# Optimization experiments

Measured on AMD Instinct MI355X. Metric: run time of the kernel, lower is better.

Reference implementation:

```python
import jax, jax.numpy as jnp
import numpy as np

B, N, M = 4, 4096, 1024
QUERY_DIM, CONTEXT_DIM = 1024, 768
HEADS, DIM_HEAD = 16, 64
INNER = HEADS * DIM_HEAD  # 1024


def setup_inputs() -> dict:
    key = jax.random.key(0)
    ks = jax.random.split(key, 7)
    s_q = 1.0 / np.sqrt(QUERY_DIM)
    s_c = 1.0 / np.sqrt(CONTEXT_DIM)
    s_i = 1.0 / np.sqrt(INNER)
    return {
        "x": jax.random.normal(ks[0], (B, N, QUERY_DIM), dtype=jnp.float32),
        "context": jax.random.normal(ks[1], (B, M, CONTEXT_DIM), dtype=jnp.float32),
        # weights stored [in, out] so y = x @ W (equiv to torch Linear with W.T)
        "Wq": jax.random.uniform(ks[2], (QUERY_DIM, INNER), minval=-s_q, maxval=s_q, dtype=jnp.float32),
        "Wk": jax.random.uniform(ks[3], (CONTEXT_DIM, INNER), minval=-s_c, maxval=s_c, dtype=jnp.float32),
        "Wv": jax.random.uniform(ks[4], (CONTEXT_DIM, INNER), minval=-s_c, maxval=s_c, dtype=jnp.float32),
        "Wo": jax.random.uniform(ks[5], (INNER, QUERY_DIM), minval=-s_i, maxval=s_i, dtype=jnp.float32),
        "bo": jax.random.uniform(ks[6], (QUERY_DIM,), minval=-s_i, maxval=s_i, dtype=jnp.float32),
    }


def reference(x, context, Wq, Wk, Wv, Wo, bo):
    scale = DIM_HEAD ** -0.5
    b, n, _ = x.shape
    m = context.shape[1]
    # projections, then split heads: [B, H, S, Dh]
    q = (x @ Wq).reshape(b, n, HEADS, DIM_HEAD).transpose(0, 2, 1, 3)
    k = (context @ Wk).reshape(b, m, HEADS, DIM_HEAD).transpose(0, 2, 1, 3)
    v = (context @ Wv).reshape(b, m, HEADS, DIM_HEAD).transpose(0, 2, 1, 3)
    sim = jnp.einsum('bhid,bhjd->bhij', q, k) * scale  # [B,H,N,M]
    attn = jax.nn.softmax(sim, axis=-1)
    out = jnp.einsum('bhij,bhjd->bhid', attn, v)       # [B,H,N,Dh]
    out = out.transpose(0, 2, 1, 3).reshape(b, n, INNER)
    return out @ Wo + bo
```

## Files before the change

kernel.cpp:

```cpp
#include <hip/hip_runtime.h>
#include <hip/hip_bf16.h>

typedef unsigned short u16;
typedef __attribute__((ext_vector_type(8))) short short8;
typedef __attribute__((ext_vector_type(4))) float f32x4;
typedef __attribute__((ext_vector_type(16))) float f32x16;
typedef __attribute__((ext_vector_type(2))) unsigned uint2v;

#define ATT_B 4
#define ATT_N 4096
#define ATT_M 1024
#define ATT_H 16
#define CBLK 64
#define NT (ATT_M / CBLK)

__device__ inline u16 f2bf(float f) {
  union { float f; unsigned u; } x; x.f = f;
  unsigned r = x.u + 0x7fffu + ((x.u >> 16) & 1u);
  return (u16)(r >> 16);
}

__device__ inline unsigned pk_bf16(float lo, float hi) {
  unsigned r;
  asm("v_cvt_pk_bf16_f32 %0, %1, %2" : "=v"(r) : "v"(lo), "v"(hi));
  return r;
}

__device__ inline float exp2_raw(float x) {
  float r;
  asm("v_exp_f32 %0, %1" : "=v"(r) : "v"(x));
  return r;
}

__device__ inline void gload_lds16(const u16* g, u16* l) {
  __builtin_amdgcn_global_load_lds(
      (const __attribute__((address_space(1))) void*)g,
      (__attribute__((address_space(3))) void*)l, 16, 0, 0);
}

__global__ __launch_bounds__(256) void prep_kernel(
    const float* __restrict__ x, u16* __restrict__ xb, int n4x,
    const float* __restrict__ ctx, u16* __restrict__ cb, int n4c,
    const float* __restrict__ Wq, const float* __restrict__ Wk,
    const float* __restrict__ Wv, const float* __restrict__ Wo,
    u16* __restrict__ wqt, u16* __restrict__ wkt,
    u16* __restrict__ wvt, u16* __restrict__ wot) {
  const int blk = blockIdx.x;
  const int tid = threadIdx.x;
  if (blk < 4096) {
    const int z = blk >> 10;
    const float* W = (z == 0) ? Wq : (z == 1) ? Wk : (z == 2) ? Wv : Wo;
    u16* Wt = (z == 0) ? wqt : (z == 1) ? wkt : (z == 2) ? wvt : wot;
    const int K = (z == 0 || z == 3) ? 1024 : 768;
    const int k0 = ((blk >> 5) & 31) * 32;
    if (k0 >= K) return;
    const int n0 = (blk & 31) * 32;
    __shared__ float T[32][33];
    const int tx = tid & 31, ty = tid >> 5;
#pragma unroll
    for (int i = 0; i < 4; ++i)
      T[ty + i * 8][tx] = W[(size_t)(k0 + ty + i * 8) * 1024 + n0 + tx];
    __syncthreads();
#pragma unroll
    for (int i = 0; i < 4; ++i)
      Wt[(size_t)(n0 + ty + i * 8) * K + k0 + tx] = f2bf(T[tx][ty + i * 8]);
  } else {
    int i = (blk - 4096) * 256 + tid;
    const float* src;
    u16* dst;
    if (i < n4x) {
      src = x; dst = xb;
    } else {
      i -= n4x;
      if (i >= n4c) return;
      src = ctx; dst = cb;
    }
    const float4 v = reinterpret_cast<const float4*>(src)[i];
    uint2 o;
    o.x = pk_bf16(v.x, v.y);
    o.y = pk_bf16(v.z, v.w);
    reinterpret_cast<uint2*>(dst)[i] = o;
  }
}

template <int F32OUT>
__device__ __forceinline__ void gemm_body(const u16* __restrict__ A,
                                          const u16* __restrict__ Bt,
                                          u16* __restrict__ Cb,
                                          float* __restrict__ Cf,
                                          const float* __restrict__ bias,
                                          float scale, int N, int K,
                                          unsigned orig, unsigned gx, unsigned nwg,
                                          u16* As, u16* Bs) {
  const int tid = threadIdx.x;
  const int lane = tid & 63;
  const int w = tid >> 6;
  const int lr = lane & 15;
  const int lk = lane >> 4;
  const int wm = w >> 1, wn = w & 1;

  const unsigned cpx = nwg >> 3;
  const unsigned swz = (orig & 7u) * cpx + (orig >> 3);
  const int brow = (int)(swz / gx) * 128;
  const int bcol = (int)(swz % gx) * 128;

  const int gr = lane >> 3;
  const int gc = (lane & 7) ^ gr;

  f32x4 acc[4][4];
#pragma unroll
  for (int mi = 0; mi < 4; ++mi)
#pragma unroll
    for (int ni = 0; ni < 4; ++ni) acc[mi][ni] = f32x4{0.f, 0.f, 0.f, 0.f};

  for (int k0 = 0; k0 < K; k0 += 64) {
#pragma unroll
    for (int i = 0; i < 4; ++i) {
      const int g = w * 4 + i;
      gload_lds16(A + (size_t)(brow + g * 8 + gr) * K + k0 + gc * 8, &As[g * 512]);
      gload_lds16(Bt + (size_t)(bcol + g * 8 + gr) * K + k0 + gc * 8, &Bs[g * 512]);
    }
    __syncthreads();
    short8 a[4][2], bb[4][2];
#pragma unroll
    for (int mi = 0; mi < 4; ++mi) {
      const int row = wm * 64 + mi * 16 + lr;
#pragma unroll
      for (int kk = 0; kk < 2; ++kk)
        a[mi][kk] = *reinterpret_cast<const short8*>(
            &As[row * 64 + (((kk * 4 + lk) ^ (lr & 7)) * 8)]);
    }
#pragma unroll
    for (int ni = 0; ni < 4; ++ni) {
      const int row = wn * 64 + ni * 16 + lr;
#pragma unroll
      for (int kk = 0; kk < 2; ++kk)
        bb[ni][kk] = *reinterpret_cast<const short8*>(
            &Bs[row * 64 + (((kk * 4 + lk) ^ (lr & 7)) * 8)]);
    }
#pragma unroll
    for (int mi = 0; mi < 4; ++mi)
#pragma unroll
      for (int ni = 0; ni < 4; ++ni)
#pragma unroll
        for (int kk = 0; kk < 2; ++kk)
          acc[mi][ni] = __builtin_amdgcn_mfma_f32_16x16x32_bf16(
              a[mi][kk], bb[ni][kk], acc[mi][ni], 0, 0, 0);
    __syncthreads();
  }

#pragma unroll
  for (int mi = 0; mi < 4; ++mi)
#pragma unroll
    for (int ni = 0; ni < 4; ++ni)
#pragma unroll
      for (int r = 0; r < 4; ++r) {
        const size_t row = (size_t)(brow + wm * 64 + mi * 16 + lk * 4 + r);
        const int col = bcol + wn * 64 + ni * 16 + lr;
        if (F32OUT)
          Cf[row * N + col] = acc[mi][ni][r] + bias[col];
        else
          Cb[row * N + col] = f2bf(acc[mi][ni][r] * scale);
      }
}

__global__ __launch_bounds__(256) void proj_kv(
    const u16* __restrict__ cb, const u16* __restrict__ wkt, u16* __restrict__ Kb,
    const u16* __restrict__ wvt, u16* __restrict__ VTb) {
  __shared__ u16 As[128 * 64];
  __shared__ u16 Bs[128 * 64];
  const unsigned blk = blockIdx.x;
  if (blk < 256)
    gemm_body<0>(cb, wkt, Kb, nullptr, nullptr, 1.0f, 1024, 768,
                 blk, 8u, 256u, As, Bs);
  else
    gemm_body<0>(wvt, cb, VTb, nullptr, nullptr, 1.0f, 4096, 768,
                 blk - 256u, 32u, 256u, As, Bs);
}

template <int F32OUT>
__global__ __launch_bounds__(512, 2) void gemm8(const u16* __restrict__ A,
                                                const u16* __restrict__ Bt,
                                                u16* __restrict__ Cb,
                                                float* __restrict__ Cf,
                                                const float* __restrict__ bias,
                                                float scale, int N, int K) {
  __shared__ u16 As[2][16384];
  __shared__ u16 Bs[2][16384];
  const int tid = threadIdx.x;
  const int lane = tid & 63;
  const int w = tid >> 6;
  const int lr = lane & 15;
  const int lk = lane >> 4;
  const int wm = w >> 2, wn = w & 3;
  const int gr = lane >> 3;
  const int gc = (lane & 7) ^ gr;

  const unsigned gx = gridDim.x;
  const unsigned nwg = gx * gridDim.y;
  const unsigned orig = blockIdx.y * gx + blockIdx.x;
  const unsigned cpx = nwg >> 3;
  const unsigned swz = (orig & 7u) * cpx + (orig >> 3);
  const int brow = (int)(swz / gx) * 256;
  const int bcol = (int)(swz % gx) * 256;

  int ag[2][2];
#pragma unroll
  for (int p = 0; p < 2; ++p)
#pragma unroll
    for (int j = 0; j < 2; ++j) {
      const int i = 2 * w + j;
      const int q = 2 * p + (i >> 3);
      const int wi = i & 7;
      ag[p][j] = (wi < 4) ? (4 * q + wi) : (16 + 4 * q + (wi - 4));
    }

#define G8_SA(d, kt, g) \
  gload_lds16(A + (size_t)(brow + (g) * 8 + gr) * K + (kt) * 64 + gc * 8, &As[d][(g) * 512])
#define G8_SB(d, kt, g) \
  gload_lds16(Bt + (size_t)(bcol + (g) * 8 + gr) * K + (kt) * 64 + gc * 8, &Bs[d][(g) * 512])

  f32x4 acc[8][4];
#pragma unroll
  for (int m = 0; m < 8; ++m)
#pragma unroll
    for (int n = 0; n < 4; ++n) acc[m][n] = f32x4{0.f, 0.f, 0.f, 0.f};

  const int NKT = K >> 6;

  G8_SB(0, 0, 4 * w + 0); G8_SB(0, 0, 4 * w + 1);
  G8_SB(0, 0, 4 * w + 2); G8_SB(0, 0, 4 * w + 3);
  G8_SA(0, 0, ag[0][0]); G8_SA(0, 0, ag[0][1]);
  G8_SA(0, 0, ag[1][0]); G8_SA(0, 0, ag[1][1]);

  for (int t = 0; t < NKT; ++t) {
    const int cur = t & 1, nxt = cur ^ 1;
    const bool pf = (t + 1) < NKT;
    const int kt1 = t + 1;
    short8 bfr[4][2];
#pragma unroll
    for (int q = 0; q < 4; ++q) {
      if (q == 0) {
        asm volatile("s_waitcnt vmcnt(2)" ::: "memory");
        __builtin_amdgcn_s_barrier();
        asm volatile("" ::: "memory");
      } else if (q == 2) {
        if (pf) asm volatile("s_waitcnt vmcnt(4)" ::: "memory");
        else    asm volatile("s_waitcnt vmcnt(0)" ::: "memory");
        __builtin_amdgcn_s_barrier();
        asm volatile("" ::: "memory");
      }
      short8 afr[2][2];
#pragma unroll
      for (int j = 0; j < 2; ++j) {
        const int row = wm * 128 + (2 * q + j) * 16 + lr;
#pragma unroll
        for (int kk = 0; kk < 2; ++kk)
          afr[j][kk] = *reinterpret_cast<const short8*>(
              &As[cur][row * 64 + (((kk * 4 + lk) ^ (lr & 7)) * 8)]);
      }
      if (q == 0) {
#pragma unroll
        for (int n = 0; n < 4; ++n) {
          const int row = wn * 64 + n * 16 + lr;
#pragma unroll
          for (int kk = 0; kk < 2; ++kk)
            bfr[n][kk] = *reinterpret_cast<const short8*>(
                &Bs[cur][row * 64 + (((kk * 4 + lk) ^ (lr & 7)) * 8)]);
        }
      }
      if (pf) {
        if (q == 0)      { G8_SB(nxt, kt1, 4 * w + 0); G8_SB(nxt, kt1, 4 * w + 1); }
        else if (q == 1) { G8_SB(nxt, kt1, 4 * w + 2); G8_SB(nxt, kt1, 4 * w + 3); }
        else if (q == 2) { G8_SA(nxt, kt1, ag[0][0]);  G8_SA(nxt, kt1, ag[0][1]); }
        else             { G8_SA(nxt, kt1, ag[1][0]);  G8_SA(nxt, kt1, ag[1][1]); }
      }
      __builtin_amdgcn_s_setprio(1);
#pragma unroll
      for (int j = 0; j < 2; ++j)
#pragma unroll
        for (int n = 0; n < 4; ++n)
#pragma unroll
          for (int kk = 0; kk < 2; ++kk)
            acc[2 * q + j][n] = __builtin_amdgcn_mfma_f32_16x16x32_bf16(
                afr[j][kk], bfr[n][kk], acc[2 * q + j][n], 0, 0, 0);
      __builtin_amdgcn_s_setprio(0);
    }
  }
#undef G8_SA
#undef G8_SB

#pragma unroll
  for (int m = 0; m < 8; ++m)
#pragma unroll
    for (int n = 0; n < 4; ++n)
#pragma unroll
      for (int r = 0; r < 4; ++r) {
        const size_t row = (size_t)(brow + wm * 128 + m * 16 + lk * 4 + r);
        const int col = bcol + wn * 64 + n * 16 + lr;
        if (F32OUT)
          Cf[row * N + col] = acc[m][n][r] + bias[col];
        else
          Cb[row * N + col] = f2bf(acc[m][n][r] * scale);
      }
}

__global__ __launch_bounds__(512, 4) void attn_kernel(const u16* __restrict__ Qg,
                                                      const u16* __restrict__ Kg,
                                                      const u16* __restrict__ VTg,
                                                      u16* __restrict__ AO) {
  __shared__ u16 Ks[2][8][512];
  __shared__ u16 Vs[2][8][512];
  __shared__ float lsw[8][32];

  const int tid = threadIdx.x;
  const int lane = tid & 63;
  const int w = tid >> 6;
  const int l = lane & 31;
  const int hi = lane >> 5;
  const int qt = blockIdx.x;
  const int bh = blockIdx.y;
  const int b = bh >> 4, h = bh & 15;
  const int qbase = qt * 256 + w * 32;

  short8 qf[4];
#pragma unroll
  for (int kc = 0; kc < 4; ++kc)
    qf[kc] = *reinterpret_cast<const short8*>(
        Qg + (size_t)(b * ATT_N + qbase + l) * 1024 + h * 64 + kc * 16 + hi * 8);

  const u16* ksrc = Kg + (size_t)(b * ATT_M + (w >> 2) * 32 + l) * 1024 + h * 64 + (w & 3) * 16 + hi * 8;
  const u16* vsrc = VTg + (size_t)(h * 64 + (w >> 2) * 32 + l) * (ATT_B * ATT_M) + b * ATT_M + (w & 3) * 16 + hi * 8;

  f32x16 Oacc[2];
  float sA = 0.f, sB = 0.f;
#pragma unroll
  for (int r = 0; r < 16; ++r) { Oacc[0][r] = 0.f; Oacc[1][r] = 0.f; }

  gload_lds16(ksrc, &Ks[0][w][0]);
  gload_lds16(vsrc, &Vs[0][w][0]);
  __syncthreads();

  int buf = 0;
  for (int t = 0; t < NT; ++t) {
    if (t + 1 < NT) {
      gload_lds16(ksrc + (size_t)(t + 1) * CBLK * 1024, &Ks[buf ^ 1][w][0]);
      gload_lds16(vsrc + (size_t)(t + 1) * CBLK, &Vs[buf ^ 1][w][0]);
    }

    f32x16 st[2];
#pragma unroll
    for (int r = 0; r < 16; ++r) { st[0][r] = 0.f; st[1][r] = 0.f; }
    __builtin_amdgcn_s_setprio(1);
#pragma unroll
    for (int ci = 0; ci < 2; ++ci)
#pragma unroll
      for (int kc = 0; kc < 4; ++kc) {
        short8 kb = *reinterpret_cast<const short8*>(&Ks[buf][ci * 4 + kc][lane * 8]);
        st[ci] = __builtin_amdgcn_mfma_f32_32x32x16_bf16(kb, qf[kc], st[ci], 0, 0, 0);
      }
    __builtin_amdgcn_s_setprio(0);

    short8 pa[4];
    float p[2][16];
#pragma unroll
    for (int ci = 0; ci < 2; ++ci) {
#pragma unroll
      for (int r = 0; r < 16; ++r) p[ci][r] = exp2_raw(st[ci][r]);
      unsigned Y0 = pk_bf16(p[ci][0], p[ci][1]),   Y1 = pk_bf16(p[ci][2], p[ci][3]);
      unsigned Y2 = pk_bf16(p[ci][4], p[ci][5]),   Y3 = pk_bf16(p[ci][6], p[ci][7]);
      unsigned Y4 = pk_bf16(p[ci][8], p[ci][9]),   Y5 = pk_bf16(p[ci][10], p[ci][11]);
      unsigned Y6 = pk_bf16(p[ci][12], p[ci][13]), Y7 = pk_bf16(p[ci][14], p[ci][15]);
      uint2v s02 = __builtin_amdgcn_permlane32_swap(Y0, Y2, false, false);
      uint2v s13 = __builtin_amdgcn_permlane32_swap(Y1, Y3, false, false);
      uint2v s46 = __builtin_amdgcn_permlane32_swap(Y4, Y6, false, false);
      uint2v s57 = __builtin_amdgcn_permlane32_swap(Y5, Y7, false, false);
      union { unsigned u[4]; short8 s; } f0, f1;
      f0.u[0] = s02.x; f0.u[1] = s13.x; f0.u[2] = s02.y; f0.u[3] = s13.y;
      f1.u[0] = s46.x; f1.u[1] = s57.x; f1.u[2] = s46.y; f1.u[3] = s57.y;
      pa[ci * 2 + 0] = f0.s;
      pa[ci * 2 + 1] = f1.s;
    }

    __builtin_amdgcn_s_setprio(1);
#pragma unroll
    for (int kcc = 0; kcc < 4; ++kcc) {
#pragma unroll
      for (int dj = 0; dj < 2; ++dj) {
        short8 vb = *reinterpret_cast<const short8*>(&Vs[buf][dj * 4 + kcc][lane * 8]);
        Oacc[dj] = __builtin_amdgcn_mfma_f32_32x32x16_bf16(pa[kcc], vb, Oacc[dj], 0, 0, 0);
      }
#pragma unroll
      for (int j = 0; j < 4; ++j) {
        sA += p[0][kcc * 4 + j];
        sB += p[1][kcc * 4 + j];
      }
    }
    __builtin_amdgcn_s_setprio(0);

    __syncthreads();
    buf ^= 1;
  }

  float lsum = sA + sB;
  lsum += __shfl_xor(lsum, 32);
  if (hi == 0) lsw[w][l] = lsum;
  __syncthreads();
#pragma unroll
  for (int r = 0; r < 16; ++r) {
    const int crow = (r & 3) + 8 * (r >> 2) + 4 * hi;
    const float inv = __builtin_amdgcn_rcpf(lsw[w][crow]);
    const size_t row = (size_t)(b * ATT_N + qbase + crow);
#pragma unroll
    for (int dj = 0; dj < 2; ++dj)
      AO[row * 1024 + h * 64 + dj * 32 + l] = f2bf(Oacc[dj][r] * inv);
  }
}

extern "C" void kernel_launch(void* const* d_in, const int* in_sizes, int n_in,
                              void* d_out, int out_size, void* d_ws, size_t ws_size,
                              hipStream_t stream) {
  const float* x   = (const float*)d_in[0];
  const float* ctx = (const float*)d_in[1];
  const float* Wq  = (const float*)d_in[2];
  const float* Wk  = (const float*)d_in[3];
  const float* Wv  = (const float*)d_in[4];
  const float* Wo  = (const float*)d_in[5];
  const float* bo  = (const float*)d_in[6];
  float* out = (float*)d_out;

  char* ws = (char*)d_ws;
  u16* xb  = (u16*)(ws);
  u16* cb  = (u16*)(ws + 33554432);
  u16* wqt = (u16*)(ws + 39845888);
  u16* wkt = (u16*)(ws + 41943040);
  u16* wvt = (u16*)(ws + 43515904);
  u16* wot = (u16*)(ws + 45088768);
  u16* Qb  = (u16*)(ws + 47185920);
  u16* Kb  = (u16*)(ws + 80740352);
  u16* VTb = (u16*)(ws + 89128960);
  u16* AOb = xb;

  prep_kernel<<<23552, 256, 0, stream>>>(x, xb, 4194304, ctx, cb, 786432,
                                         Wq, Wk, Wv, Wo, wqt, wkt, wvt, wot);

  const float qscale = 0.125f * 1.44269504088896f;
  gemm8<0><<<dim3(4, 64), 512, 0, stream>>>(xb, wqt, Qb, nullptr, nullptr, qscale, 1024, 1024);
  proj_kv<<<512, 256, 0, stream>>>(cb, wkt, Kb, wvt, VTb);

  attn_kernel<<<dim3(16, 64), 512, 0, stream>>>(Qb, Kb, VTb, AOb);

  gemm8<1><<<dim3(4, 64), 512, 0, stream>>>(AOb, wot, nullptr, out, bo, 1.0f, 1024, 1024);
}
```

Baseline: 192.3 us.

## Fuse Q, K and V projections into one 256x256-tile GEMM launch

Merges the Q projection GEMM and the separate K/V projection kernel into a single launch of 384 blocks that dispatch on block index to Q, K or V^T work. The K/V work moves from the 128x128 single-buffered gemm_body onto the pipelined 256x256 double-buffered gemm8 body. The aim is to cut one kernel launch and its tail, and to use the more efficient pipelined tile for K/V. In exchange K and V^T now get only 64 blocks each at the larger tile, so the work is coarser and load balance across blocks may suffer.

```diff
diff --git a/kernel.cpp b/kernel.cpp
--- a/kernel.cpp
+++ b/kernel.cpp
@@ -84,109 +84,14 @@
 }
 
 template <int F32OUT>
-__device__ __forceinline__ void gemm_body(const u16* __restrict__ A,
-                                          const u16* __restrict__ Bt,
-                                          u16* __restrict__ Cb,
-                                          float* __restrict__ Cf,
-                                          const float* __restrict__ bias,
-                                          float scale, int N, int K,
-                                          unsigned orig, unsigned gx, unsigned nwg,
-                                          u16* As, u16* Bs) {
-  const int tid = threadIdx.x;
-  const int lane = tid & 63;
-  const int w = tid >> 6;
-  const int lr = lane & 15;
-  const int lk = lane >> 4;
-  const int wm = w >> 1, wn = w & 1;
-
-  const unsigned cpx = nwg >> 3;
-  const unsigned swz = (orig & 7u) * cpx + (orig >> 3);
-  const int brow = (int)(swz / gx) * 128;
-  const int bcol = (int)(swz % gx) * 128;
-
-  const int gr = lane >> 3;
-  const int gc = (lane & 7) ^ gr;
-
-  f32x4 acc[4][4];
-#pragma unroll
-  for (int mi = 0; mi < 4; ++mi)
-#pragma unroll
-    for (int ni = 0; ni < 4; ++ni) acc[mi][ni] = f32x4{0.f, 0.f, 0.f, 0.f};
-
-  for (int k0 = 0; k0 < K; k0 += 64) {
-#pragma unroll
-    for (int i = 0; i < 4; ++i) {
-      const int g = w * 4 + i;
-      gload_lds16(A + (size_t)(brow + g * 8 + gr) * K + k0 + gc * 8, &As[g * 512]);
-      gload_lds16(Bt + (size_t)(bcol + g * 8 + gr) * K + k0 + gc * 8, &Bs[g * 512]);
-    }
-    __syncthreads();
-    short8 a[4][2], bb[4][2];
-#pragma unroll
-    for (int mi = 0; mi < 4; ++mi) {
-      const int row = wm * 64 + mi * 16 + lr;
-#pragma unroll
-      for (int kk = 0; kk < 2; ++kk)
-        a[mi][kk] = *reinterpret_cast<const short8*>(
-            &As[row * 64 + (((kk * 4 + lk) ^ (lr & 7)) * 8)]);
-    }
-#pragma unroll
-    for (int ni = 0; ni < 4; ++ni) {
-      const int row = wn * 64 + ni * 16 + lr;
-#pragma unroll
-      for (int kk = 0; kk < 2; ++kk)
-        bb[ni][kk] = *reinterpret_cast<const short8*>(
-            &Bs[row * 64 + (((kk * 4 + lk) ^ (lr & 7)) * 8)]);
-    }
-#pragma unroll
-    for (int mi = 0; mi < 4; ++mi)
-#pragma unroll
-      for (int ni = 0; ni < 4; ++ni)
-#pragma unroll
-        for (int kk = 0; kk < 2; ++kk)
-          acc[mi][ni] = __builtin_amdgcn_mfma_f32_16x16x32_bf16(
-              a[mi][kk], bb[ni][kk], acc[mi][ni], 0, 0, 0);
-    __syncthreads();
-  }
-
-#pragma unroll
-  for (int mi = 0; mi < 4; ++mi)
-#pragma unroll
-    for (int ni = 0; ni < 4; ++ni)
-#pragma unroll
-      for (int r = 0; r < 4; ++r) {
-        const size_t row = (size_t)(brow + wm * 64 + mi * 16 + lk * 4 + r);
-        const int col = bcol + wn * 64 + ni * 16 + lr;
-        if (F32OUT)
-          Cf[row * N + col] = acc[mi][ni][r] + bias[col];
-        else
-          Cb[row * N + col] = f2bf(acc[mi][ni][r] * scale);
-      }
-}
-
-__global__ __launch_bounds__(256) void proj_kv(
-    const u16* __restrict__ cb, const u16* __restrict__ wkt, u16* __restrict__ Kb,
-    const u16* __restrict__ wvt, u16* __restrict__ VTb) {
-  __shared__ u16 As[128 * 64];
-  __shared__ u16 Bs[128 * 64];
-  const unsigned blk = blockIdx.x;
-  if (blk < 256)
-    gemm_body<0>(cb, wkt, Kb, nullptr, nullptr, 1.0f, 1024, 768,
-                 blk, 8u, 256u, As, Bs);
-  else
-    gemm_body<0>(wvt, cb, VTb, nullptr, nullptr, 1.0f, 4096, 768,
-                 blk - 256u, 32u, 256u, As, Bs);
-}
-
-template <int F32OUT>
-__global__ __launch_bounds__(512, 2) void gemm8(const u16* __restrict__ A,
-                                                const u16* __restrict__ Bt,
-                                                u16* __restrict__ Cb,
-                                                float* __restrict__ Cf,
-                                                const float* __restrict__ bias,
-                                                float scale, int N, int K) {
-  __shared__ u16 As[2][16384];
-  __shared__ u16 Bs[2][16384];
+__device__ __forceinline__ void gemm8_body(const u16* __restrict__ A,
+                                           const u16* __restrict__ Bt,
+                                           u16* __restrict__ Cb,
+                                           float* __restrict__ Cf,
+                                           const float* __restrict__ bias,
+                                           float scale, int N, int K,
+                                           unsigned orig, unsigned gx, unsigned nwg,
+                                           u16* AsL, u16* BsL) {
   const int tid = threadIdx.x;
   const int lane = tid & 63;
   const int w = tid >> 6;
@@ -196,9 +101,6 @@
   const int gr = lane >> 3;
   const int gc = (lane & 7) ^ gr;
 
-  const unsigned gx = gridDim.x;
-  const unsigned nwg = gx * gridDim.y;
-  const unsigned orig = blockIdx.y * gx + blockIdx.x;
   const unsigned cpx = nwg >> 3;
   const unsigned swz = (orig & 7u) * cpx + (orig >> 3);
   const int brow = (int)(swz / gx) * 256;
@@ -216,9 +118,9 @@
     }
 
 #define G8_SA(d, kt, g) \
-  gload_lds16(A + (size_t)(brow + (g) * 8 + gr) * K + (kt) * 64 + gc * 8, &As[d][(g) * 512])
+  gload_lds16(A + (size_t)(brow + (g) * 8 + gr) * K + (kt) * 64 + gc * 8, &AsL[(d) * 16384 + (g) * 512])
 #define G8_SB(d, kt, g) \
-  gload_lds16(Bt + (size_t)(bcol + (g) * 8 + gr) * K + (kt) * 64 + gc * 8, &Bs[d][(g) * 512])
+  gload_lds16(Bt + (size_t)(bcol + (g) * 8 + gr) * K + (kt) * 64 + gc * 8, &BsL[(d) * 16384 + (g) * 512])
 
   f32x4 acc[8][4];
 #pragma unroll
@@ -257,7 +159,7 @@
 #pragma unroll
         for (int kk = 0; kk < 2; ++kk)
           afr[j][kk] = *reinterpret_cast<const short8*>(
-              &As[cur][row * 64 + (((kk * 4 + lk) ^ (lr & 7)) * 8)]);
+              &AsL[cur * 16384 + row * 64 + (((kk * 4 + lk) ^ (lr & 7)) * 8)]);
       }
       if (q == 0) {
 #pragma unroll
@@ -266,7 +168,7 @@
 #pragma unroll
           for (int kk = 0; kk < 2; ++kk)
             bfr[n][kk] = *reinterpret_cast<const short8*>(
-                &Bs[cur][row * 64 + (((kk * 4 + lk) ^ (lr & 7)) * 8)]);
+                &BsL[cur * 16384 + row * 64 + (((kk * 4 + lk) ^ (lr & 7)) * 8)]);
         }
       }
       if (pf) {
@@ -303,6 +205,38 @@
         else
           Cb[row * N + col] = f2bf(acc[m][n][r] * scale);
       }
+}
+
+__global__ __launch_bounds__(512, 2) void proj_all(
+    const u16* __restrict__ xb, const u16* __restrict__ wqt, u16* __restrict__ Qb,
+    float qscale,
+    const u16* __restrict__ cb, const u16* __restrict__ wkt, u16* __restrict__ Kb,
+    const u16* __restrict__ wvt, u16* __restrict__ VTb) {
+  __shared__ u16 As[2][16384];
+  __shared__ u16 Bs[2][16384];
+  const unsigned blk = blockIdx.x;
+  if (blk < 256)
+    gemm8_body<0>(xb, wqt, Qb, nullptr, nullptr, qscale, 1024, 1024,
+                  blk, 4u, 256u, &As[0][0], &Bs[0][0]);
+  else if (blk < 320)
+    gemm8_body<0>(cb, wkt, Kb, nullptr, nullptr, 1.0f, 1024, 768,
+                  blk - 256u, 4u, 64u, &As[0][0], &Bs[0][0]);
+  else
+    gemm8_body<0>(wvt, cb, VTb, nullptr, nullptr, 1.0f, 4096, 768,
+                  blk - 320u, 16u, 64u, &As[0][0], &Bs[0][0]);
+}
+
+__global__ __launch_bounds__(512, 2) void gemm8_out(const u16* __restrict__ A,
+                                                    const u16* __restrict__ Bt,
+                                                    float* __restrict__ Cf,
+                                                    const float* __restrict__ bias) {
+  __shared__ u16 As[2][16384];
+  __shared__ u16 Bs[2][16384];
+  const unsigned gx = gridDim.x;
+  const unsigned nwg = gx * gridDim.y;
+  const unsigned orig = blockIdx.y * gx + blockIdx.x;
+  gemm8_body<1>(A, Bt, nullptr, Cf, bias, 1.0f, 1024, 1024,
+                orig, gx, nwg, &As[0][0], &Bs[0][0]);
 }
 
 __global__ __launch_bounds__(512, 4) void attn_kernel(const u16* __restrict__ Qg,
@@ -445,10 +379,9 @@
                                          Wq, Wk, Wv, Wo, wqt, wkt, wvt, wot);
 
   const float qscale = 0.125f * 1.44269504088896f;
-  gemm8<0><<<dim3(4, 64), 512, 0, stream>>>(xb, wqt, Qb, nullptr, nullptr, qscale, 1024, 1024);
-  proj_kv<<<512, 256, 0, stream>>>(cb, wkt, Kb, wvt, VTb);
+  proj_all<<<384, 512, 0, stream>>>(xb, wqt, Qb, qscale, cb, wkt, Kb, wvt, VTb);
 
   attn_kernel<<<dim3(16, 64), 512, 0, stream>>>(Qb, Kb, VTb, AOb);
 
-  gemm8<1><<<dim3(4, 64), 512, 0, stream>>>(AOb, wot, nullptr, out, bo, 1.0f, 1024, 1024);
-}
+  gemm8_out<<<dim3(4, 64), 512, 0, stream>>>(AOb, wot, out, bo);
+}
```

Measured after the change: 187.7 us, median of 2. -2.4%, faster.
